# Optimization experiments

Measured on AMD Instinct MI355X. Metric: run time of the kernel, lower is better.

Reference implementation:

```python
import jax, jax.numpy as jnp
import numpy as np

B = 4096
FEAT = 512
EMB = 64
HID = 1024
NUM_CLASSES = 64   # == option_num == noise_lib_Y.shape[0]
LIB_X = 256
LIB_Y = 256
OUT_J = 256


def setup_inputs() -> dict:
    key = jax.random.key(0)
    ks = jax.random.split(key, 16)
    s = lambda k, shape, fan: jax.random.normal(k, shape, jnp.float32) / np.sqrt(fan)
    d_in = FEAT + EMB
    return {
        "state": jax.random.normal(ks[0], (B, FEAT), jnp.float32),
        "option": jax.random.randint(ks[1], (B,), 0, NUM_CLASSES, jnp.int64),
        "embed_table": s(ks[2], (NUM_CLASSES, EMB), EMB),
        "Wx1": s(ks[3], (d_in, HID), d_in), "bx1": jnp.zeros((HID,), jnp.float32),
        "Wx2": s(ks[4], (HID, LIB_X), HID), "bx2": jnp.zeros((LIB_X,), jnp.float32),
        "Wy1": s(ks[5], (d_in, HID), d_in), "by1": jnp.zeros((HID,), jnp.float32),
        "Wy2": s(ks[6], (HID, LIB_Y), HID), "by2": jnp.zeros((LIB_Y,), jnp.float32),
        "noise_lib_X": s(ks[7], (LIB_X, OUT_J), LIB_X),
        "noise_lib_Y": s(ks[8], (NUM_CLASSES, LIB_Y, OUT_J), LIB_Y),
    }


def _mlp(x, W1, b1, W2, b2):
    # MLP_RELU, layer_num=2: Linear -> ReLU -> Linear
    h = jax.nn.relu(x @ W1 + b1)
    return h @ W2 + b2


def reference(state, option, embed_table, Wx1, bx1, Wx2, bx2,
              Wy1, by1, Wy2, by2, noise_lib_X, noise_lib_Y):
    option_embed = embed_table[option]                      # [B, EMB]
    all_state = jnp.concatenate([state, option_embed], axis=-1)
    cls_X = _mlp(all_state, Wx1, bx1, Wx2, bx2)             # [B, LIB_X]
    cls_Y = _mlp(all_state, Wy1, by1, Wy2, by2)             # [B, LIB_Y]
    # Original: einsum('bi,mij->bmj') then mask with one_hot(option).
    # Mathematically identical gather-then-matmul (honors the routing sparsity):
    noise_Y_sel = noise_lib_Y[option]                       # [B, LIB_Y, OUT_J]
    generate_noise_Y = jnp.einsum('bi,bij->bj', cls_Y, noise_Y_sel)
    generate_noise_X = cls_X @ noise_lib_X                  # [B, OUT_J]
    return (generate_noise_X, generate_noise_Y)
```

## Files before the change

### kernel.cpp

```cpp
#include <hip/hip_runtime.h>

typedef unsigned short u16;
typedef unsigned int u32;

using f32x4  = __attribute__((ext_vector_type(4))) float;
using bf16x8 = __attribute__((ext_vector_type(8))) __bf16;

#define DEV __device__ __forceinline__

DEV u16 f2bf(float f) {
  union { float f; u32 u; } x; x.f = f;
  return (u16)((x.u + 0x7fffu + ((x.u >> 16) & 1u)) >> 16);
}
DEV float bf2f(u16 h) {
  union { u32 u; float f; } x; x.u = ((u32)h) << 16;
  return x.f;
}

DEV void async_cp16(const u16* g, u16* l) {
  __builtin_amdgcn_global_load_lds((const __attribute__((address_space(1))) void*)g,
                                   (__attribute__((address_space(3))) void*)l,
                                   16, 0, 0);
}

static constexpr int BATCH = 4096;
static constexpr int FEAT  = 512;
static constexpr int EMB   = 64;
static constexpr int HID   = 1024;
static constexpr int NC    = 64;
static constexpr int DIN   = 576;
static constexpr int LIB   = 256;

DEV void detect_lite(const u32* __restrict__ sraw, const u32* __restrict__ oraw,
                     int* isf32, int* ostr) {
  __shared__ int cib, conz;
  const int t = threadIdx.x;
  if (t == 0) { cib = 0; conz = 0; }
  u32 w = sraw[t];
  u32 e = (w >> 7) & 0xFFu;
  unsigned long long m1 = __ballot(e >= 100 && e <= 142);
  unsigned long long m2 = __ballot((t & 1) && oraw[t] != 0);
  __syncthreads();
  if ((t & 63) == 0) {
    atomicAdd(&cib, __popcll(m1));
    atomicAdd(&conz, __popcll(m2));
  }
  __syncthreads();
  *isf32 = (cib < 128) ? 1 : 0;
  *ostr  = (conz == 0) ? 2 : 1;
}

DEV void load16_bf(u16* v, const void* __restrict__ in, size_t off, int isf32) {
  if (isf32) {
    const float4* s = (const float4*)((const float*)in + off);
    float4 a0 = s[0], a1 = s[1], a2 = s[2], a3 = s[3];
    v[0] = f2bf(a0.x); v[1] = f2bf(a0.y); v[2]  = f2bf(a0.z); v[3]  = f2bf(a0.w);
    v[4] = f2bf(a1.x); v[5] = f2bf(a1.y); v[6]  = f2bf(a1.z); v[7]  = f2bf(a1.w);
    v[8] = f2bf(a2.x); v[9] = f2bf(a2.y); v[10] = f2bf(a2.z); v[11] = f2bf(a2.w);
    v[12] = f2bf(a3.x); v[13] = f2bf(a3.y); v[14] = f2bf(a3.z); v[15] = f2bf(a3.w);
  } else {
    const uint4* s = (const uint4*)((const u16*)in + off);
    *(uint4*)&v[0] = s[0];
    *(uint4*)&v[8] = s[1];
  }
}

DEV void do_transpose64(u16* lds, const void* __restrict__ in,
                        u16* __restrict__ out, int R, int C,
                        int by, int bx, int isf32) {
  u16* tile = lds;
  const int t = threadIdx.x;
  {
    const int r = t >> 2, c0 = (t & 3) * 16;
    u16 v[16];
    load16_bf(v, in, (size_t)(by * 64 + r) * C + (bx * 64 + c0), isf32);
    *(uint4*)&tile[r * 72 + c0]     = *(uint4*)&v[0];
    *(uint4*)&tile[r * 72 + c0 + 8] = *(uint4*)&v[8];
  }
  __syncthreads();
  {
    const int c = t & 63, rs = (t >> 6) * 16;
    u16 w[16];
#pragma unroll
    for (int i = 0; i < 16; ++i) w[i] = tile[(rs + i) * 72 + c];
    size_t oo = (size_t)(bx * 64 + c) * R + (by * 64 + rs);
    *(uint4*)&out[oo]     = *(uint4*)&w[0];
    *(uint4*)&out[oo + 8] = *(uint4*)&w[8];
  }
}

DEV void tgemm_task(u16* lds, const void* __restrict__ nX,
                    const void* __restrict__ Wx2, u16* __restrict__ T,
                    int mt, int nt, int isf32) {
  u16* Als = lds;
  u16* Bls = lds + 64 * 72;
  const int t = threadIdx.x;
  const int m0 = mt * 64, q0 = nt * 64;
  const int lane = t & 63, wid = t >> 6;
  const int wm = wid >> 1, wn = wid & 1;
  const int lr = lane & 15, lq = lane >> 4;
  f32x4 acc[2][2] = {};
  for (int k0 = 0; k0 < LIB; k0 += 64) {
    __syncthreads();
    {
      const int r = t >> 2, c0 = (t & 3) * 16;
      u16 v[16];
      load16_bf(v, nX, (size_t)(k0 + r) * LIB + m0 + c0, isf32);
#pragma unroll
      for (int j = 0; j < 16; ++j) Als[(c0 + j) * 72 + r] = v[j];
      const int q = t >> 2, ic = (t & 3) * 16;
      u16 w16[16];
      load16_bf(w16, Wx2, (size_t)(q0 + q) * LIB + k0 + ic, isf32);
      u16* dst = &Bls[((ic >> 5) * 64 + q) * 32 + (ic & 31)];
      *(uint4*)dst       = *(uint4*)&w16[0];
      *(uint4*)(dst + 8) = *(uint4*)&w16[8];
    }
    __syncthreads();
#pragma unroll
    for (int sl = 0; sl < 2; ++sl) {
      bf16x8 av[2], bv[2];
#pragma unroll
      for (int i2 = 0; i2 < 2; ++i2)
        av[i2] = *(const bf16x8*)&Als[(wm * 32 + i2 * 16 + lr) * 72 + sl * 32 + lq * 8];
#pragma unroll
      for (int j2 = 0; j2 < 2; ++j2)
        bv[j2] = *(const bf16x8*)&Bls[(sl * 64 + wn * 32 + j2 * 16 + lr) * 32 + lq * 8];
#pragma unroll
      for (int i2 = 0; i2 < 2; ++i2)
#pragma unroll
        for (int j2 = 0; j2 < 2; ++j2)
          acc[i2][j2] = __builtin_amdgcn_mfma_f32_16x16x32_bf16(av[i2], bv[j2], acc[i2][j2], 0, 0, 0);
    }
  }
#pragma unroll
  for (int j2 = 0; j2 < 2; ++j2) {
    const int gc = q0 + wn * 32 + j2 * 16 + lr;
#pragma unroll
    for (int i2 = 0; i2 < 2; ++i2) {
      const int gr = m0 + wm * 32 + i2 * 16 + lq * 4;
#pragma unroll
      for (int r = 0; r < 4; ++r)
        T[(size_t)(gr + r) * HID + gc] = f2bf(acc[i2][j2][r]);
    }
  }
}

struct PrepArgs {
  const void *state, *emb, *Wx1, *Wy1;
  const int* opt;
  u16 *all_state, *WT1x, *WT1y;
};
static constexpr int PB_CONCAT = BATCH * 36 / 256;
static constexpr int PB_WT1 = (DIN / 64) * (HID / 64);
static constexpr int PREP_BLOCKS = PB_CONCAT + 2 * PB_WT1;

__global__ __launch_bounds__(256) void prep_k(PrepArgs a) {
  __shared__ __align__(16) u16 plds[64 * 72];
  int isf32, os;
  detect_lite((const u32*)a.state, (const u32*)a.opt, &isf32, &os);
  int bid = blockIdx.x;
  const int t = threadIdx.x;
  if (bid < PB_CONCAT) {
    int idx = bid * 256 + t;
    int b = idx / 36, ch = idx % 36;
    const void* base;
    size_t srcoff;
    if (ch < 32) { base = a.state; srcoff = (size_t)b * FEAT + ch * 16; }
    else {
      base = a.emb;
      srcoff = (size_t)a.opt[(size_t)b * os] * EMB + (ch - 32) * 16;
    }
    u16 o[16];
    load16_bf(o, base, srcoff, isf32);
    u16* dst = a.all_state + (size_t)b * DIN + ch * 16;
    *(uint4*)dst       = *(const uint4*)&o[0];
    *(uint4*)(dst + 8) = *(const uint4*)&o[8];
    return;
  }
  bid -= PB_CONCAT;
  if (bid < PB_WT1) { do_transpose64(plds, a.Wx1, a.WT1x, DIN, HID, bid >> 4, bid & 15, isf32); return; }
  bid -= PB_WT1;
  do_transpose64(plds, a.Wy1, a.WT1y, DIN, HID, bid >> 4, bid & 15, isf32);
}

template <int BM, int BN, int SLABS, bool RELU>
DEV void gemm_tile(u16* lds, const u16* __restrict__ A, const u16* __restrict__ Bt,
                   const void* bias, void* C, int N, int K, int m0, int n0,
                   int isf32, bool cf32, bool bf32) {
  constexpr int WM = BM / 2, WN = BN / 2, TM = WM / 16, TN = WN / 16;
  u16* As = lds;
  u16* Bs = lds + BM * 32 * SLABS;
  const int t = threadIdx.x;
  const int lane = t & 63, wid = t >> 6;
  const int wm = wid >> 1, wn = wid & 1;
  const int lr = lane & 15, lq = lane >> 4;
  f32x4 acc[TM][TN] = {};
  for (int k0 = 0; k0 < K; k0 += 32 * SLABS) {
    __syncthreads();
#pragma unroll
    for (int sl = 0; sl < SLABS; ++sl) {
#pragma unroll
      for (int u = 0; u < BM / 64; ++u) {
        int unit = u * 256 + t;
        int r = unit >> 2, c8 = (unit & 3) * 8;
        async_cp16(A + (size_t)(m0 + r) * K + (k0 + sl * 32 + c8),
                   &As[(sl * BM + r) * 32 + c8]);
      }
#pragma unroll
      for (int u = 0; u < BN / 64; ++u) {
        int unit = u * 256 + t;
        int r = unit >> 2, c8 = (unit & 3) * 8;
        async_cp16(Bt + (size_t)(n0 + r) * K + (k0 + sl * 32 + c8),
                   &Bs[(sl * BN + r) * 32 + c8]);
      }
    }
    __syncthreads();
#pragma unroll
    for (int sl = 0; sl < SLABS; ++sl) {
      bf16x8 av[TM], bv[TN];
#pragma unroll
      for (int i = 0; i < TM; ++i)
        av[i] = *(const bf16x8*)&As[(sl * BM + wm * WM + i * 16 + lr) * 32 + lq * 8];
#pragma unroll
      for (int j = 0; j < TN; ++j)
        bv[j] = *(const bf16x8*)&Bs[(sl * BN + wn * WN + j * 16 + lr) * 32 + lq * 8];
#pragma unroll
      for (int i = 0; i < TM; ++i)
#pragma unroll
        for (int j = 0; j < TN; ++j)
          acc[i][j] = __builtin_amdgcn_mfma_f32_16x16x32_bf16(av[i], bv[j], acc[i][j], 0, 0, 0);
    }
  }
#pragma unroll
  for (int j = 0; j < TN; ++j) {
    const int gc = n0 + wn * WN + j * 16 + lr;
    const float bval = bias
        ? (bf32 ? ((const float*)bias)[gc] : bf2f(((const u16*)bias)[gc]))
        : 0.f;
#pragma unroll
    for (int i = 0; i < TM; ++i) {
      const int gr = m0 + wm * WM + i * 16 + lq * 4;
#pragma unroll
      for (int r = 0; r < 4; ++r) {
        float v = acc[i][j][r] + bval;
        if (RELU) v = fmaxf(v, 0.f);
        const size_t idx = (size_t)(gr + r) * N + gc;
        if (cf32) ((float*)C)[idx] = v;
        else      ((u16*)C)[idx] = f2bf(v);
      }
    }
  }
}

struct G1Args {
  const u16 *all_state, *WT1x, *WT1y;
  const void *bx1, *by1, *Wy2, *nX, *Wx2, *bx2, *state, *opt;
  u16 *h_x, *h_y, *WT2y, *T;
  float* b2x;
};
static constexpr int G1_GEMM = 1024;
static constexpr int G1_BLOCKS = G1_GEMM + 64 + 64 + 4;

__global__ __launch_bounds__(256) void gemm1_k(G1Args a) {
  __shared__ __align__(16) u16 lds[(128 + 64) * 96];
  __shared__ float red[4][64];
  int isf32, os;
  detect_lite((const u32*)a.state, (const u32*)a.opt, &isf32, &os);
  int bid = blockIdx.x;
  const int t = threadIdx.x;
  if (bid < G1_GEMM) {
    const int x = bid & 15, y = (bid >> 4) & 31, z = bid >> 9;
    gemm_tile<128, 64, 3, true>(lds,
        a.all_state, z ? a.WT1y : a.WT1x, z ? a.by1 : a.bx1,
        z ? a.h_y : a.h_x, HID, DIN, y * 128, x * 64, isf32, false, isf32);
    return;
  }
  bid -= G1_GEMM;
  if (bid < 64) { do_transpose64(lds, a.Wy2, a.WT2y, HID, LIB, bid >> 2, bid & 3, isf32); return; }
  bid -= 64;
  if (bid < 64) { tgemm_task(lds, a.nX, a.Wx2, a.T, bid & 3, bid >> 2, isf32); return; }
  bid -= 64;
  {
    const int j = bid * 64 + (t & 63), g = t >> 6;
    float acc = 0.f;
    for (int ii = 0; ii < 64; ++ii) {
      const int i = g * 64 + ii;
      float s = isf32 ? ((const float*)a.bx2)[i] : bf2f(((const u16*)a.bx2)[i]);
      float v = isf32 ? ((const float*)a.nX)[(size_t)i * LIB + j]
                      : bf2f(((const u16*)a.nX)[(size_t)i * LIB + j]);
      acc += s * v;
    }
    red[g][t & 63] = acc;
    __syncthreads();
    if (g == 0)
      a.b2x[j] = red[0][t & 63] + red[1][t & 63] + red[2][t & 63] + red[3][t & 63];
  }
}

struct GArg { const u16* A; const u16* Bt; const void* bias; void* C; int cflag; int bflag; };

template <int BM, int BN, int SLABS, bool RELU>
__global__ __launch_bounds__(256) void gemm_bt(GArg g0, GArg g1, int N, int K,
                                               const void* state, const void* opt) {
  __shared__ __align__(16) u16 lds[(BM + BN) * 32 * SLABS];
  int isf32, os;
  detect_lite((const u32*)state, (const u32*)opt, &isf32, &os);
  const GArg g = blockIdx.z ? g1 : g0;
  gemm_tile<BM, BN, SLABS, RELU>(lds, g.A, g.Bt, g.bias, g.C, N, K,
                                 blockIdx.y * BM, blockIdx.x * BN,
                                 isf32, g.cflag && isf32, g.bflag || isf32);
}

struct TailArgs {
  const u16* cls_y;
  const void *nY, *state;
  const int* opt;
  void* out;
};

__global__ __launch_bounds__(256) void tail_k(TailArgs a) {
  __shared__ __align__(16) u16 lds[25216];
  __shared__ int lcnt;
  int isf32, os;
  detect_lite((const u32*)a.state, (const u32*)a.opt, &isf32, &os);
  const bool of32 = (isf32 != 0);
  const int t = threadIdx.x;
  const int lane = t & 63, w = t >> 6, lr = lane & 15, lq = lane >> 4;

  u16* Bts  = lds;
  u16* Asm  = lds + 16896;
  u16* list = lds + 21120;
  const int m = blockIdx.x >> 3;
  const int n0 = ((blockIdx.x >> 1) & 3) * 64;
  const int half = blockIdx.x & 1;
  if (t == 0) lcnt = 0;

#pragma unroll
  for (int pass = 0; pass < 4; ++pass) {
    const int k = pass * 64 + (t >> 2), nc = (t & 3) * 16;
    u16 v[16];
    load16_bf(v, a.nY, ((size_t)m * LIB + k) * LIB + n0 + nc, isf32);
#pragma unroll
    for (int j = 0; j < 16; ++j) Bts[(nc + j) * 264 + k] = v[j];
  }

  __syncthreads();
  const int bstart = half * (BATCH / 2), bend = bstart + BATCH / 2;
  for (int base = bstart; base < bend; base += 256) {
    const int b = base + t;
    const int e = a.opt[(size_t)b * os];
    unsigned long long mk = __ballot(e == m);
    const int nw = __popcll(mk);
    int wbase = 0;
    if (lane == 0 && nw) wbase = atomicAdd(&lcnt, nw);
    wbase = __shfl(wbase, 0);
    const int mypre = __popcll(mk & ((1ull << lane) - 1ull));
    if (e == m) list[wbase + mypre] = (u16)b;
  }
  __syncthreads();
  const int cnt = lcnt;
  const size_t out_off = (size_t)BATCH * LIB;

  for (int ch = 0; ch < cnt; ch += 16) {
    __syncthreads();
    {
      const int r = t >> 4, cb = (t & 15) * 16;
      if (ch + r < cnt) {
        const u16* src = a.cls_y + (size_t)list[ch + r] * LIB + cb;
        *(uint4*)&Asm[r * 264 + cb]     = *(const uint4*)src;
        *(uint4*)&Asm[r * 264 + cb + 8] = *(const uint4*)(src + 8);
      } else {
        uint4 z{0, 0, 0, 0};
        *(uint4*)&Asm[r * 264 + cb]     = z;
        *(uint4*)&Asm[r * 264 + cb + 8] = z;
      }
    }
    __syncthreads();
    f32x4 acc = {};
#pragma unroll
    for (int kk = 0; kk < LIB; kk += 32) {
      bf16x8 av = *(const bf16x8*)&Asm[lr * 264 + kk + lq * 8];
      bf16x8 bv = *(const bf16x8*)&Bts[(w * 16 + lr) * 264 + kk + lq * 8];
      acc = __builtin_amdgcn_mfma_f32_16x16x32_bf16(av, bv, acc, 0, 0, 0);
    }
#pragma unroll
    for (int r = 0; r < 4; ++r) {
      const int rowc = lq * 4 + r;
      if (ch + rowc < cnt) {
        const size_t oi = out_off + (size_t)list[ch + rowc] * LIB
                        + (n0 + w * 16 + lr);
        if (of32) ((float*)a.out)[oi] = acc[r];
        else      ((u16*)a.out)[oi] = f2bf(acc[r]);
      }
    }
  }
}

extern "C" void kernel_launch(void* const* d_in, const int* in_sizes, int n_in,
                              void* d_out, int out_size, void* d_ws, size_t ws_size,
                              hipStream_t stream) {
  char* p = (char*)d_ws;
  auto alloc = [&](size_t bytes) { char* r = p; p += (bytes + 255) & ~(size_t)255; return r; };
  u16* all_state = (u16*)alloc((size_t)BATCH * DIN * 2);
  u16* h_x   = (u16*)alloc((size_t)BATCH * HID * 2);
  u16* h_y   = (u16*)alloc((size_t)BATCH * HID * 2);
  u16* cls_y = (u16*)alloc((size_t)BATCH * LIB * 2);
  u16* WT1x  = (u16*)alloc((size_t)HID * DIN * 2);
  u16* WT1y  = (u16*)alloc((size_t)HID * DIN * 2);
  u16* WT2y  = (u16*)alloc((size_t)LIB * HID * 2);
  u16* T     = (u16*)alloc((size_t)LIB * HID * 2);
  float* b2x = (float*)alloc((size_t)LIB * 4);

  const void* state = d_in[0];
  const void* opt   = d_in[1];

  PrepArgs pa;
  pa.state = state; pa.opt = (const int*)opt; pa.emb = d_in[2];
  pa.Wx1 = d_in[3]; pa.Wy1 = d_in[7];
  pa.all_state = all_state; pa.WT1x = WT1x; pa.WT1y = WT1y;
  prep_k<<<PREP_BLOCKS, 256, 0, stream>>>(pa);

  G1Args g1;
  g1.all_state = all_state; g1.WT1x = WT1x; g1.WT1y = WT1y;
  g1.bx1 = d_in[4]; g1.by1 = d_in[8];
  g1.Wy2 = d_in[9]; g1.nX = d_in[11]; g1.Wx2 = d_in[5]; g1.bx2 = d_in[6];
  g1.state = state; g1.opt = opt;
  g1.h_x = h_x; g1.h_y = h_y; g1.WT2y = WT2y; g1.T = T; g1.b2x = b2x;
  gemm1_k<<<G1_BLOCKS, 256, 0, stream>>>(g1);

  GArg g2x{h_x, T, b2x, d_out, 1, 1};
  GArg g2y{h_y, WT2y, d_in[10], cls_y, 0, 0};
  gemm_bt<64, 64, 4, false><<<dim3(LIB / 64, BATCH / 64, 2), 256, 0, stream>>>(
      g2x, g2y, LIB, HID, state, opt);

  TailArgs ta{cls_y, d_in[12], state, (const int*)opt, d_out};
  tail_k<<<512, 256, 0, stream>>>(ta);
}
```

Measured before the change: 147.7 us.

## Double-buffer GEMM LDS staging, widen gemm1 tiles, pad tail LDS stride

The shared GEMM tile routine now uses two LDS buffers, so the async global-to-LDS copies for the next K slab are issued before the MFMA work on the current slab, with one barrier per iteration instead of two. The first-layer GEMM moves from 128x64 tiles with 3 slabs to 128x128 tiles with 2 slabs, halving its block count and raising reuse per block. The tail kernel's LDS row stride changes from 264 to 266 elements to reduce bank conflicts. In exchange, LDS use per block roughly doubles, which can cut occupancy, and the 266 stride leaves rows that are not 16-byte aligned for the 128-bit LDS accesses.

```diff
diff --git a/kernel.cpp b/kernel.cpp
--- a/kernel.cpp
+++ b/kernel.cpp
@@ -188,15 +188,15 @@
                    const void* bias, void* C, int N, int K, int m0, int n0,
                    int isf32, bool cf32, bool bf32) {
   constexpr int WM = BM / 2, WN = BN / 2, TM = WM / 16, TN = WN / 16;
-  u16* As = lds;
-  u16* Bs = lds + BM * 32 * SLABS;
+  constexpr int BUFE = (BM + BN) * 32 * SLABS;
   const int t = threadIdx.x;
   const int lane = t & 63, wid = t >> 6;
   const int wm = wid >> 1, wn = wid & 1;
   const int lr = lane & 15, lq = lane >> 4;
-  f32x4 acc[TM][TN] = {};
-  for (int k0 = 0; k0 < K; k0 += 32 * SLABS) {
-    __syncthreads();
+
+  auto stage = [&](int buf, int k0) {
+    u16* As = lds + buf * BUFE;
+    u16* Bs = As + BM * 32 * SLABS;
 #pragma unroll
     for (int sl = 0; sl < SLABS; ++sl) {
 #pragma unroll
@@ -214,7 +214,17 @@
                    &Bs[(sl * BN + r) * 32 + c8]);
       }
     }
-    __syncthreads();
+  };
+
+  f32x4 acc[TM][TN] = {};
+  stage(0, 0);
+  __syncthreads();
+  int cur = 0;
+  for (int k0 = 0; k0 < K; k0 += 32 * SLABS) {
+    const int kn = k0 + 32 * SLABS;
+    if (kn < K) stage(cur ^ 1, kn);
+    const u16* As = lds + cur * BUFE;
+    const u16* Bs = As + BM * 32 * SLABS;
 #pragma unroll
     for (int sl = 0; sl < SLABS; ++sl) {
       bf16x8 av[TM], bv[TN];
@@ -230,6 +240,8 @@
         for (int j = 0; j < TN; ++j)
           acc[i][j] = __builtin_amdgcn_mfma_f32_16x16x32_bf16(av[i], bv[j], acc[i][j], 0, 0, 0);
     }
+    __syncthreads();
+    cur ^= 1;
   }
 #pragma unroll
   for (int j = 0; j < TN; ++j) {
@@ -258,21 +270,21 @@
   u16 *h_x, *h_y, *WT2y, *T;
   float* b2x;
 };
-static constexpr int G1_GEMM = 1024;
+static constexpr int G1_GEMM = 512;
 static constexpr int G1_BLOCKS = G1_GEMM + 64 + 64 + 4;
 
 __global__ __launch_bounds__(256) void gemm1_k(G1Args a) {
-  __shared__ __align__(16) u16 lds[(128 + 64) * 96];
+  __shared__ __align__(16) u16 lds[2 * (128 + 128) * 32 * 2];
   __shared__ float red[4][64];
   int isf32, os;
   detect_lite((const u32*)a.state, (const u32*)a.opt, &isf32, &os);
   int bid = blockIdx.x;
   const int t = threadIdx.x;
   if (bid < G1_GEMM) {
-    const int x = bid & 15, y = (bid >> 4) & 31, z = bid >> 9;
-    gemm_tile<128, 64, 3, true>(lds,
+    const int x = bid & 7, y = (bid >> 3) & 31, z = bid >> 8;
+    gemm_tile<128, 128, 2, true>(lds,
         a.all_state, z ? a.WT1y : a.WT1x, z ? a.by1 : a.bx1,
-        z ? a.h_y : a.h_x, HID, DIN, y * 128, x * 64, isf32, false, isf32);
+        z ? a.h_y : a.h_x, HID, DIN, y * 128, x * 128, isf32, false, isf32);
     return;
   }
   bid -= G1_GEMM;
@@ -302,7 +314,7 @@
 template <int BM, int BN, int SLABS, bool RELU>
 __global__ __launch_bounds__(256) void gemm_bt(GArg g0, GArg g1, int N, int K,
                                                const void* state, const void* opt) {
-  __shared__ __align__(16) u16 lds[(BM + BN) * 32 * SLABS];
+  __shared__ __align__(16) u16 lds[2 * (BM + BN) * 32 * SLABS];
   int isf32, os;
   detect_lite((const u32*)state, (const u32*)opt, &isf32, &os);
   const GArg g = blockIdx.z ? g1 : g0;
@@ -318,6 +330,8 @@
   void* out;
 };
 
+static constexpr int TSTR = 266;
+
 __global__ __launch_bounds__(256) void tail_k(TailArgs a) {
   __shared__ __align__(16) u16 lds[25216];
   __shared__ int lcnt;
@@ -328,8 +342,8 @@
   const int lane = t & 63, w = t >> 6, lr = lane & 15, lq = lane >> 4;
 
   u16* Bts  = lds;
-  u16* Asm  = lds + 16896;
-  u16* list = lds + 21120;
+  u16* Asm  = lds + 64 * TSTR;
+  u16* list = lds + 80 * TSTR;
   const int m = blockIdx.x >> 3;
   const int n0 = ((blockIdx.x >> 1) & 3) * 64;
   const int half = blockIdx.x & 1;
@@ -341,7 +355,7 @@
     u16 v[16];
     load16_bf(v, a.nY, ((size_t)m * LIB + k) * LIB + n0 + nc, isf32);
 #pragma unroll
-    for (int j = 0; j < 16; ++j) Bts[(nc + j) * 264 + k] = v[j];
+    for (int j = 0; j < 16; ++j) Bts[(nc + j) * TSTR + k] = v[j];
   }
 
   __syncthreads();
@@ -367,20 +381,20 @@
       const int r = t >> 4, cb = (t & 15) * 16;
       if (ch + r < cnt) {
         const u16* src = a.cls_y + (size_t)list[ch + r] * LIB + cb;
-        *(uint4*)&Asm[r * 264 + cb]     = *(const uint4*)src;
-        *(uint4*)&Asm[r * 264 + cb + 8] = *(const uint4*)(src + 8);
+        *(uint4*)&Asm[r * TSTR + cb]     = *(const uint4*)src;
+        *(uint4*)&Asm[r * TSTR + cb + 8] = *(const uint4*)(src + 8);
       } else {
         uint4 z{0, 0, 0, 0};
-        *(uint4*)&Asm[r * 264 + cb]     = z;
-        *(uint4*)&Asm[r * 264 + cb + 8] = z;
+        *(uint4*)&Asm[r * TSTR + cb]     = z;
+        *(uint4*)&Asm[r * TSTR + cb + 8] = z;
       }
     }
     __syncthreads();
     f32x4 acc = {};
 #pragma unroll
     for (int kk = 0; kk < LIB; kk += 32) {
-      bf16x8 av = *(const bf16x8*)&Asm[lr * 264 + kk + lq * 8];
-      bf16x8 bv = *(const bf16x8*)&Bts[(w * 16 + lr) * 264 + kk + lq * 8];
+      bf16x8 av = *(const bf16x8*)&Asm[lr * TSTR + kk + lq * 8];
+      bf16x8 bv = *(const bf16x8*)&Bts[(w * 16 + lr) * TSTR + kk + lq * 8];
       acc = __builtin_amdgcn_mfma_f32_16x16x32_bf16(av, bv, acc, 0, 0, 0);
     }
 #pragma unroll
```

After: 159.4 us. +7.9%, slower.

## Split-K second-layer GEMMs into fp32 partials and reduce them in the tail kernel

Applied to the files above, without the earlier changes.

The second-layer GEMMs for both heads are split along K into two halves, doubling the grid to raise occupancy. Each half writes fp32 partials to a new workspace buffer. The tail kernel gains extra blocks that sum the X partials, add the bias and write the output. The Y path sums its partials, adds by2 and converts to bf16 when staging rows for the routed matmul, and the LDS row stride changes from 264 to 266. The cost is an extra 16 MB of fp32 partial traffic and the extra reduction work.

```diff
diff --git a/kernel.cpp b/kernel.cpp
--- a/kernel.cpp
+++ b/kernel.cpp
@@ -186,7 +186,7 @@
 template <int BM, int BN, int SLABS, bool RELU>
 DEV void gemm_tile(u16* lds, const u16* __restrict__ A, const u16* __restrict__ Bt,
                    const void* bias, void* C, int N, int K, int m0, int n0,
-                   int isf32, bool cf32, bool bf32) {
+                   int kbeg, int kend, int isf32, bool cf32, bool bf32) {
   constexpr int WM = BM / 2, WN = BN / 2, TM = WM / 16, TN = WN / 16;
   u16* As = lds;
   u16* Bs = lds + BM * 32 * SLABS;
@@ -195,7 +195,7 @@
   const int wm = wid >> 1, wn = wid & 1;
   const int lr = lane & 15, lq = lane >> 4;
   f32x4 acc[TM][TN] = {};
-  for (int k0 = 0; k0 < K; k0 += 32 * SLABS) {
+  for (int k0 = kbeg; k0 < kend; k0 += 32 * SLABS) {
     __syncthreads();
 #pragma unroll
     for (int sl = 0; sl < SLABS; ++sl) {
@@ -272,7 +272,8 @@
     const int x = bid & 15, y = (bid >> 4) & 31, z = bid >> 9;
     gemm_tile<128, 64, 3, true>(lds,
         a.all_state, z ? a.WT1y : a.WT1x, z ? a.by1 : a.bx1,
-        z ? a.h_y : a.h_x, HID, DIN, y * 128, x * 64, isf32, false, isf32);
+        z ? a.h_y : a.h_x, HID, DIN, y * 128, x * 64, 0, DIN,
+        isf32, false, isf32 != 0);
     return;
   }
   bid -= G1_GEMM;
@@ -297,26 +298,35 @@
   }
 }
 
-struct GArg { const u16* A; const u16* Bt; const void* bias; void* C; int cflag; int bflag; };
-
-template <int BM, int BN, int SLABS, bool RELU>
-__global__ __launch_bounds__(256) void gemm_bt(GArg g0, GArg g1, int N, int K,
-                                               const void* state, const void* opt) {
-  __shared__ __align__(16) u16 lds[(BM + BN) * 32 * SLABS];
+struct G2Args {
+  const u16 *h_x, *h_y, *T, *WT2y;
+  float* part;
+  const void *state, *opt;
+};
+
+__global__ __launch_bounds__(256) void gemm2_k(G2Args a) {
+  __shared__ __align__(16) u16 lds[(64 + 64) * 32 * 4];
   int isf32, os;
-  detect_lite((const u32*)state, (const u32*)opt, &isf32, &os);
-  const GArg g = blockIdx.z ? g1 : g0;
-  gemm_tile<BM, BN, SLABS, RELU>(lds, g.A, g.Bt, g.bias, g.C, N, K,
-                                 blockIdx.y * BM, blockIdx.x * BN,
-                                 isf32, g.cflag && isf32, g.bflag || isf32);
+  detect_lite((const u32*)a.state, (const u32*)a.opt, &isf32, &os);
+  const int head = blockIdx.z >> 1, half = blockIdx.z & 1;
+  const u16* A  = head ? a.h_y : a.h_x;
+  const u16* Bt = head ? a.WT2y : a.T;
+  float* C = a.part + (size_t)blockIdx.z * BATCH * LIB;
+  const int kbeg = half * (HID / 2);
+  gemm_tile<64, 64, 4, false>(lds, A, Bt, nullptr, C, LIB, HID,
+                              blockIdx.y * 64, blockIdx.x * 64,
+                              kbeg, kbeg + HID / 2, isf32, true, true);
 }
 
 struct TailArgs {
-  const u16* cls_y;
-  const void *nY, *state;
+  const float* part;
+  const void *nY, *state, *by2;
+  const float* b2x;
   const int* opt;
   void* out;
 };
+
+static constexpr int TSTR = 266;
 
 __global__ __launch_bounds__(256) void tail_k(TailArgs a) {
   __shared__ __align__(16) u16 lds[25216];
@@ -325,23 +335,64 @@
   detect_lite((const u32*)a.state, (const u32*)a.opt, &isf32, &os);
   const bool of32 = (isf32 != 0);
   const int t = threadIdx.x;
+
+  if (blockIdx.x >= 512) {
+    const int cb = blockIdx.x - 512;
+    const size_t e0 = ((size_t)cb * 256 + t) * 16;
+    const float4* s0 = (const float4*)(a.part + e0);
+    const float4* s1 = (const float4*)(a.part + (size_t)BATCH * LIB + e0);
+    const int c0 = (int)(e0 & 255);
+    float v[16];
+#pragma unroll
+    for (int q = 0; q < 4; ++q) {
+      float4 x0 = s0[q], x1 = s1[q];
+      v[q * 4 + 0] = x0.x + x1.x + a.b2x[c0 + q * 4 + 0];
+      v[q * 4 + 1] = x0.y + x1.y + a.b2x[c0 + q * 4 + 1];
+      v[q * 4 + 2] = x0.z + x1.z + a.b2x[c0 + q * 4 + 2];
+      v[q * 4 + 3] = x0.w + x1.w + a.b2x[c0 + q * 4 + 3];
+    }
+    if (of32) {
+      float4* d = (float4*)((float*)a.out + e0);
+#pragma unroll
+      for (int q = 0; q < 4; ++q) d[q] = make_float4(v[q*4], v[q*4+1], v[q*4+2], v[q*4+3]);
+    } else {
+      u16 o[16];
+#pragma unroll
+      for (int j = 0; j < 16; ++j) o[j] = f2bf(v[j]);
+      u16* d = (u16*)a.out + e0;
+      *(uint4*)d       = *(const uint4*)&o[0];
+      *(uint4*)(d + 8) = *(const uint4*)&o[8];
+    }
+    return;
+  }
+
   const int lane = t & 63, w = t >> 6, lr = lane & 15, lq = lane >> 4;
-
   u16* Bts  = lds;
-  u16* Asm  = lds + 16896;
-  u16* list = lds + 21120;
+  u16* Asm  = lds + 64 * TSTR;
+  u16* list = lds + 80 * TSTR;
   const int m = blockIdx.x >> 3;
   const int n0 = ((blockIdx.x >> 1) & 3) * 64;
   const int half = blockIdx.x & 1;
   if (t == 0) lcnt = 0;
 
+  const float* py0 = a.part + (size_t)2 * BATCH * LIB;
+  const float* py1 = a.part + (size_t)3 * BATCH * LIB;
+  float byv[16];
+  {
+    const int cb = (t & 15) * 16;
+#pragma unroll
+    for (int j = 0; j < 16; ++j)
+      byv[j] = isf32 ? ((const float*)a.by2)[cb + j]
+                     : bf2f(((const u16*)a.by2)[cb + j]);
+  }
+
 #pragma unroll
   for (int pass = 0; pass < 4; ++pass) {
     const int k = pass * 64 + (t >> 2), nc = (t & 3) * 16;
     u16 v[16];
     load16_bf(v, a.nY, ((size_t)m * LIB + k) * LIB + n0 + nc, isf32);
 #pragma unroll
-    for (int j = 0; j < 16; ++j) Bts[(nc + j) * 264 + k] = v[j];
+    for (int j = 0; j < 16; ++j) Bts[(nc + j) * TSTR + k] = v[j];
   }
 
   __syncthreads();
@@ -366,21 +417,32 @@
     {
       const int r = t >> 4, cb = (t & 15) * 16;
       if (ch + r < cnt) {
-        const u16* src = a.cls_y + (size_t)list[ch + r] * LIB + cb;
-        *(uint4*)&Asm[r * 264 + cb]     = *(const uint4*)src;
-        *(uint4*)&Asm[r * 264 + cb + 8] = *(const uint4*)(src + 8);
+        const int row = list[ch + r];
+        const float4* s0 = (const float4*)(py0 + (size_t)row * LIB + cb);
+        const float4* s1 = (const float4*)(py1 + (size_t)row * LIB + cb);
+        u16 o[16];
+#pragma unroll
+        for (int q = 0; q < 4; ++q) {
+          float4 x0 = s0[q], x1 = s1[q];
+          o[q * 4 + 0] = f2bf(x0.x + x1.x + byv[q * 4 + 0]);
+          o[q * 4 + 1] = f2bf(x0.y + x1.y + byv[q * 4 + 1]);
+          o[q * 4 + 2] = f2bf(x0.z + x1.z + byv[q * 4 + 2]);
+          o[q * 4 + 3] = f2bf(x0.w + x1.w + byv[q * 4 + 3]);
+        }
+        *(uint4*)&Asm[r * TSTR + cb]     = *(const uint4*)&o[0];
+        *(uint4*)&Asm[r * TSTR + cb + 8] = *(const uint4*)&o[8];
       } else {
         uint4 z{0, 0, 0, 0};
-        *(uint4*)&Asm[r * 264 + cb]     = z;
-        *(uint4*)&Asm[r * 264 + cb + 8] = z;
+        *(uint4*)&Asm[r * TSTR + cb]     = z;
+        *(uint4*)&Asm[r * TSTR + cb + 8] = z;
       }
     }
     __syncthreads();
     f32x4 acc = {};
 #pragma unroll
     for (int kk = 0; kk < LIB; kk += 32) {
-      bf16x8 av = *(const bf16x8*)&Asm[lr * 264 + kk + lq * 8];
-      bf16x8 bv = *(const bf16x8*)&Bts[(w * 16 + lr) * 264 + kk + lq * 8];
+      bf16x8 av = *(const bf16x8*)&Asm[lr * TSTR + kk + lq * 8];
+      bf16x8 bv = *(const bf16x8*)&Bts[(w * 16 + lr) * TSTR + kk + lq * 8];
       acc = __builtin_amdgcn_mfma_f32_16x16x32_bf16(av, bv, acc, 0, 0, 0);
     }
 #pragma unroll
@@ -404,12 +466,12 @@
   u16* all_state = (u16*)alloc((size_t)BATCH * DIN * 2);
   u16* h_x   = (u16*)alloc((size_t)BATCH * HID * 2);
   u16* h_y   = (u16*)alloc((size_t)BATCH * HID * 2);
-  u16* cls_y = (u16*)alloc((size_t)BATCH * LIB * 2);
   u16* WT1x  = (u16*)alloc((size_t)HID * DIN * 2);
   u16* WT1y  = (u16*)alloc((size_t)HID * DIN * 2);
   u16* WT2y  = (u16*)alloc((size_t)LIB * HID * 2);
   u16* T     = (u16*)alloc((size_t)LIB * HID * 2);
   float* b2x = (float*)alloc((size_t)LIB * 4);
+  float* part = (float*)alloc((size_t)4 * BATCH * LIB * 4);
 
   const void* state = d_in[0];
   const void* opt   = d_in[1];
@@ -428,11 +490,13 @@
   g1.h_x = h_x; g1.h_y = h_y; g1.WT2y = WT2y; g1.T = T; g1.b2x = b2x;
   gemm1_k<<<G1_BLOCKS, 256, 0, stream>>>(g1);
 
-  GArg g2x{h_x, T, b2x, d_out, 1, 1};
-  GArg g2y{h_y, WT2y, d_in[10], cls_y, 0, 0};
-  gemm_bt<64, 64, 4, false><<<dim3(LIB / 64, BATCH / 64, 2), 256, 0, stream>>>(
-      g2x, g2y, LIB, HID, state, opt);
-
-  TailArgs ta{cls_y, d_in[12], state, (const int*)opt, d_out};
-  tail_k<<<512, 256, 0, stream>>>(ta);
-}
+  G2Args g2;
+  g2.h_x = h_x; g2.h_y = h_y; g2.T = T; g2.WT2y = WT2y;
+  g2.part = part; g2.state = state; g2.opt = opt;
+  gemm2_k<<<dim3(LIB / 64, BATCH / 64, 4), 256, 0, stream>>>(g2);
+
+  TailArgs ta;
+  ta.part = part; ta.nY = d_in[12]; ta.state = state; ta.by2 = d_in[10];
+  ta.b2x = b2x; ta.opt = (const int*)opt; ta.out = d_out;
+  tail_k<<<768, 256, 0, stream>>>(ta);
+}
```

Result: slower. 163.2 us (+10.5%).

## Move weight prep tasks into prep kernel, shrink gemm2 tiles, pad tail LDS stride

Applied to the files above, without the earlier changes.

Moves the Wy2 transpose, the nX·Wx2 product and the bias-fold work out of the first GEMM kernel into the prep kernel, leaving gemm1 as a pure GEMM grid. The second GEMM now uses 64x32 tiles, doubling its block count for better CU occupancy. The gemm_tile load loops are generalized to cover tiles smaller than 64 rows. The tail kernel's LDS row stride changes from 264 to 266 to reduce bank conflicts. This trades a larger prep kernel and smaller per-block reuse for better load balance.

```diff
diff --git a/kernel.cpp b/kernel.cpp
--- a/kernel.cpp
+++ b/kernel.cpp
@@ -146,16 +146,18 @@
 }
 
 struct PrepArgs {
-  const void *state, *emb, *Wx1, *Wy1;
+  const void *state, *emb, *Wx1, *Wy1, *Wy2, *nX, *Wx2, *bx2;
   const int* opt;
-  u16 *all_state, *WT1x, *WT1y;
+  u16 *all_state, *WT1x, *WT1y, *WT2y, *T;
+  float* b2x;
 };
 static constexpr int PB_CONCAT = BATCH * 36 / 256;
 static constexpr int PB_WT1 = (DIN / 64) * (HID / 64);
-static constexpr int PREP_BLOCKS = PB_CONCAT + 2 * PB_WT1;
+static constexpr int PREP_BLOCKS = PB_CONCAT + 2 * PB_WT1 + 64 + 64 + 4;
 
 __global__ __launch_bounds__(256) void prep_k(PrepArgs a) {
-  __shared__ __align__(16) u16 plds[64 * 72];
+  __shared__ __align__(16) u16 plds[64 * 72 + 128 * 32];
+  __shared__ float red[4][64];
   int isf32, os;
   detect_lite((const u32*)a.state, (const u32*)a.opt, &isf32, &os);
   int bid = blockIdx.x;
@@ -180,105 +182,11 @@
   bid -= PB_CONCAT;
   if (bid < PB_WT1) { do_transpose64(plds, a.Wx1, a.WT1x, DIN, HID, bid >> 4, bid & 15, isf32); return; }
   bid -= PB_WT1;
-  do_transpose64(plds, a.Wy1, a.WT1y, DIN, HID, bid >> 4, bid & 15, isf32);
-}
-
-template <int BM, int BN, int SLABS, bool RELU>
-DEV void gemm_tile(u16* lds, const u16* __restrict__ A, const u16* __restrict__ Bt,
-                   const void* bias, void* C, int N, int K, int m0, int n0,
-                   int isf32, bool cf32, bool bf32) {
-  constexpr int WM = BM / 2, WN = BN / 2, TM = WM / 16, TN = WN / 16;
-  u16* As = lds;
-  u16* Bs = lds + BM * 32 * SLABS;
-  const int t = threadIdx.x;
-  const int lane = t & 63, wid = t >> 6;
-  const int wm = wid >> 1, wn = wid & 1;
-  const int lr = lane & 15, lq = lane >> 4;
-  f32x4 acc[TM][TN] = {};
-  for (int k0 = 0; k0 < K; k0 += 32 * SLABS) {
-    __syncthreads();
-#pragma unroll
-    for (int sl = 0; sl < SLABS; ++sl) {
-#pragma unroll
-      for (int u = 0; u < BM / 64; ++u) {
-        int unit = u * 256 + t;
-        int r = unit >> 2, c8 = (unit & 3) * 8;
-        async_cp16(A + (size_t)(m0 + r) * K + (k0 + sl * 32 + c8),
-                   &As[(sl * BM + r) * 32 + c8]);
-      }
-#pragma unroll
-      for (int u = 0; u < BN / 64; ++u) {
-        int unit = u * 256 + t;
-        int r = unit >> 2, c8 = (unit & 3) * 8;
-        async_cp16(Bt + (size_t)(n0 + r) * K + (k0 + sl * 32 + c8),
-                   &Bs[(sl * BN + r) * 32 + c8]);
-      }
-    }
-    __syncthreads();
-#pragma unroll
-    for (int sl = 0; sl < SLABS; ++sl) {
-      bf16x8 av[TM], bv[TN];
-#pragma unroll
-      for (int i = 0; i < TM; ++i)
-        av[i] = *(const bf16x8*)&As[(sl * BM + wm * WM + i * 16 + lr) * 32 + lq * 8];
-#pragma unroll
-      for (int j = 0; j < TN; ++j)
-        bv[j] = *(const bf16x8*)&Bs[(sl * BN + wn * WN + j * 16 + lr) * 32 + lq * 8];
-#pragma unroll
-      for (int i = 0; i < TM; ++i)
-#pragma unroll
-        for (int j = 0; j < TN; ++j)
-          acc[i][j] = __builtin_amdgcn_mfma_f32_16x16x32_bf16(av[i], bv[j], acc[i][j], 0, 0, 0);
-    }
-  }
-#pragma unroll
-  for (int j = 0; j < TN; ++j) {
-    const int gc = n0 + wn * WN + j * 16 + lr;
-    const float bval = bias
-        ? (bf32 ? ((const float*)bias)[gc] : bf2f(((const u16*)bias)[gc]))
-        : 0.f;
-#pragma unroll
-    for (int i = 0; i < TM; ++i) {
-      const int gr = m0 + wm * WM + i * 16 + lq * 4;
-#pragma unroll
-      for (int r = 0; r < 4; ++r) {
-        float v = acc[i][j][r] + bval;
-        if (RELU) v = fmaxf(v, 0.f);
-        const size_t idx = (size_t)(gr + r) * N + gc;
-        if (cf32) ((float*)C)[idx] = v;
-        else      ((u16*)C)[idx] = f2bf(v);
-      }
-    }
-  }
-}
-
-struct G1Args {
-  const u16 *all_state, *WT1x, *WT1y;
-  const void *bx1, *by1, *Wy2, *nX, *Wx2, *bx2, *state, *opt;
-  u16 *h_x, *h_y, *WT2y, *T;
-  float* b2x;
-};
-static constexpr int G1_GEMM = 1024;
-static constexpr int G1_BLOCKS = G1_GEMM + 64 + 64 + 4;
-
-__global__ __launch_bounds__(256) void gemm1_k(G1Args a) {
-  __shared__ __align__(16) u16 lds[(128 + 64) * 96];
-  __shared__ float red[4][64];
-  int isf32, os;
-  detect_lite((const u32*)a.state, (const u32*)a.opt, &isf32, &os);
-  int bid = blockIdx.x;
-  const int t = threadIdx.x;
-  if (bid < G1_GEMM) {
-    const int x = bid & 15, y = (bid >> 4) & 31, z = bid >> 9;
-    gemm_tile<128, 64, 3, true>(lds,
-        a.all_state, z ? a.WT1y : a.WT1x, z ? a.by1 : a.bx1,
-        z ? a.h_y : a.h_x, HID, DIN, y * 128, x * 64, isf32, false, isf32);
-    return;
-  }
-  bid -= G1_GEMM;
-  if (bid < 64) { do_transpose64(lds, a.Wy2, a.WT2y, HID, LIB, bid >> 2, bid & 3, isf32); return; }
+  if (bid < PB_WT1) { do_transpose64(plds, a.Wy1, a.WT1y, DIN, HID, bid >> 4, bid & 15, isf32); return; }
+  bid -= PB_WT1;
+  if (bid < 64) { do_transpose64(plds, a.Wy2, a.WT2y, HID, LIB, bid >> 2, bid & 3, isf32); return; }
   bid -= 64;
-  if (bid < 64) { tgemm_task(lds, a.nX, a.Wx2, a.T, bid & 3, bid >> 2, isf32); return; }
+  if (bid < 64) { tgemm_task(plds, a.nX, a.Wx2, a.T, bid & 3, bid >> 2, isf32); return; }
   bid -= 64;
   {
     const int j = bid * 64 + (t & 63), g = t >> 6;
@@ -297,6 +205,91 @@
   }
 }
 
+template <int BM, int BN, int SLABS, bool RELU>
+DEV void gemm_tile(u16* lds, const u16* __restrict__ A, const u16* __restrict__ Bt,
+                   const void* bias, void* C, int N, int K, int m0, int n0,
+                   int isf32, bool cf32, bool bf32) {
+  constexpr int WM = BM / 2, WN = BN / 2, TM = WM / 16, TN = WN / 16;
+  u16* As = lds;
+  u16* Bs = lds + BM * 32 * SLABS;
+  const int t = threadIdx.x;
+  const int lane = t & 63, wid = t >> 6;
+  const int wm = wid >> 1, wn = wid & 1;
+  const int lr = lane & 15, lq = lane >> 4;
+  f32x4 acc[TM][TN] = {};
+  for (int k0 = 0; k0 < K; k0 += 32 * SLABS) {
+    __syncthreads();
+#pragma unroll
+    for (int sl = 0; sl < SLABS; ++sl) {
+#pragma unroll
+      for (int u = t; u < BM * 4; u += 256) {
+        int r = u >> 2, c8 = (u & 3) * 8;
+        async_cp16(A + (size_t)(m0 + r) * K + (k0 + sl * 32 + c8),
+                   &As[(sl * BM + r) * 32 + c8]);
+      }
+#pragma unroll
+      for (int u = t; u < BN * 4; u += 256) {
+        int r = u >> 2, c8 = (u & 3) * 8;
+        async_cp16(Bt + (size_t)(n0 + r) * K + (k0 + sl * 32 + c8),
+                   &Bs[(sl * BN + r) * 32 + c8]);
+      }
+    }
+    __syncthreads();
+#pragma unroll
+    for (int sl = 0; sl < SLABS; ++sl) {
+      bf16x8 av[TM], bv[TN];
+#pragma unroll
+      for (int i = 0; i < TM; ++i)
+        av[i] = *(const bf16x8*)&As[(sl * BM + wm * WM + i * 16 + lr) * 32 + lq * 8];
+#pragma unroll
+      for (int j = 0; j < TN; ++j)
+        bv[j] = *(const bf16x8*)&Bs[(sl * BN + wn * WN + j * 16 + lr) * 32 + lq * 8];
+#pragma unroll
+      for (int i = 0; i < TM; ++i)
+#pragma unroll
+        for (int j = 0; j < TN; ++j)
+          acc[i][j] = __builtin_amdgcn_mfma_f32_16x16x32_bf16(av[i], bv[j], acc[i][j], 0, 0, 0);
+    }
+  }
+#pragma unroll
+  for (int j = 0; j < TN; ++j) {
+    const int gc = n0 + wn * WN + j * 16 + lr;
+    const float bval = bias
+        ? (bf32 ? ((const float*)bias)[gc] : bf2f(((const u16*)bias)[gc]))
+        : 0.f;
+#pragma unroll
+    for (int i = 0; i < TM; ++i) {
+      const int gr = m0 + wm * WM + i * 16 + lq * 4;
+#pragma unroll
+      for (int r = 0; r < 4; ++r) {
+        float v = acc[i][j][r] + bval;
+        if (RELU) v = fmaxf(v, 0.f);
+        const size_t idx = (size_t)(gr + r) * N + gc;
+        if (cf32) ((float*)C)[idx] = v;
+        else      ((u16*)C)[idx] = f2bf(v);
+      }
+    }
+  }
+}
+
+struct G1Args {
+  const u16 *all_state, *WT1x, *WT1y;
+  const void *bx1, *by1, *state, *opt;
+  u16 *h_x, *h_y;
+};
+
+__global__ __launch_bounds__(256) void gemm1_k(G1Args a) {
+  __shared__ __align__(16) u16 lds[(128 + 64) * 96];
+  int isf32, os;
+  detect_lite((const u32*)a.state, (const u32*)a.opt, &isf32, &os);
+  const int bid = blockIdx.x;
+  const int x = bid & 15, y = (bid >> 4) & 31, z = bid >> 9;
+  gemm_tile<128, 64, 3, true>(lds,
+      a.all_state, z ? a.WT1y : a.WT1x, z ? a.by1 : a.bx1,
+      z ? a.h_y : a.h_x, HID, DIN, y * 128, x * 64,
+      isf32, false, isf32 != 0);
+}
+
 struct GArg { const u16* A; const u16* Bt; const void* bias; void* C; int cflag; int bflag; };
 
 template <int BM, int BN, int SLABS, bool RELU>
@@ -318,6 +311,8 @@
   void* out;
 };
 
+static constexpr int TSTR = 266;
+
 __global__ __launch_bounds__(256) void tail_k(TailArgs a) {
   __shared__ __align__(16) u16 lds[25216];
   __shared__ int lcnt;
@@ -328,8 +323,8 @@
   const int lane = t & 63, w = t >> 6, lr = lane & 15, lq = lane >> 4;
 
   u16* Bts  = lds;
-  u16* Asm  = lds + 16896;
-  u16* list = lds + 21120;
+  u16* Asm  = lds + 64 * TSTR;
+  u16* list = lds + 80 * TSTR;
   const int m = blockIdx.x >> 3;
   const int n0 = ((blockIdx.x >> 1) & 3) * 64;
   const int half = blockIdx.x & 1;
@@ -341,7 +336,7 @@
     u16 v[16];
     load16_bf(v, a.nY, ((size_t)m * LIB + k) * LIB + n0 + nc, isf32);
 #pragma unroll
-    for (int j = 0; j < 16; ++j) Bts[(nc + j) * 264 + k] = v[j];
+    for (int j = 0; j < 16; ++j) Bts[(nc + j) * TSTR + k] = v[j];
   }
 
   __syncthreads();
@@ -367,20 +362,20 @@
       const int r = t >> 4, cb = (t & 15) * 16;
       if (ch + r < cnt) {
         const u16* src = a.cls_y + (size_t)list[ch + r] * LIB + cb;
-        *(uint4*)&Asm[r * 264 + cb]     = *(const uint4*)src;
-        *(uint4*)&Asm[r * 264 + cb + 8] = *(const uint4*)(src + 8);
+        *(uint4*)&Asm[r * TSTR + cb]     = *(const uint4*)src;
+        *(uint4*)&Asm[r * TSTR + cb + 8] = *(const uint4*)(src + 8);
       } else {
         uint4 z{0, 0, 0, 0};
-        *(uint4*)&Asm[r * 264 + cb]     = z;
-        *(uint4*)&Asm[r * 264 + cb + 8] = z;
+        *(uint4*)&Asm[r * TSTR + cb]     = z;
+        *(uint4*)&Asm[r * TSTR + cb + 8] = z;
       }
     }
     __syncthreads();
     f32x4 acc = {};
 #pragma unroll
     for (int kk = 0; kk < LIB; kk += 32) {
-      bf16x8 av = *(const bf16x8*)&Asm[lr * 264 + kk + lq * 8];
-      bf16x8 bv = *(const bf16x8*)&Bts[(w * 16 + lr) * 264 + kk + lq * 8];
+      bf16x8 av = *(const bf16x8*)&Asm[lr * TSTR + kk + lq * 8];
+      bf16x8 bv = *(const bf16x8*)&Bts[(w * 16 + lr) * TSTR + kk + lq * 8];
       acc = __builtin_amdgcn_mfma_f32_16x16x32_bf16(av, bv, acc, 0, 0, 0);
     }
 #pragma unroll
@@ -417,20 +412,21 @@
   PrepArgs pa;
   pa.state = state; pa.opt = (const int*)opt; pa.emb = d_in[2];
   pa.Wx1 = d_in[3]; pa.Wy1 = d_in[7];
-  pa.all_state = all_state; pa.WT1x = WT1x; pa.WT1y = WT1y;
+  pa.Wy2 = d_in[9]; pa.nX = d_in[11]; pa.Wx2 = d_in[5]; pa.bx2 = d_in[6];
+  pa.all_state = all_state; pa.WT1x = WT1x; pa.WT1y = WT1y; pa.WT2y = WT2y;
+  pa.T = T; pa.b2x = b2x;
   prep_k<<<PREP_BLOCKS, 256, 0, stream>>>(pa);
 
   G1Args g1;
   g1.all_state = all_state; g1.WT1x = WT1x; g1.WT1y = WT1y;
   g1.bx1 = d_in[4]; g1.by1 = d_in[8];
-  g1.Wy2 = d_in[9]; g1.nX = d_in[11]; g1.Wx2 = d_in[5]; g1.bx2 = d_in[6];
   g1.state = state; g1.opt = opt;
-  g1.h_x = h_x; g1.h_y = h_y; g1.WT2y = WT2y; g1.T = T; g1.b2x = b2x;
-  gemm1_k<<<G1_BLOCKS, 256, 0, stream>>>(g1);
+  g1.h_x = h_x; g1.h_y = h_y;
+  gemm1_k<<<1024, 256, 0, stream>>>(g1);
 
   GArg g2x{h_x, T, b2x, d_out, 1, 1};
   GArg g2y{h_y, WT2y, d_in[10], cls_y, 0, 0};
-  gemm_bt<64, 64, 4, false><<<dim3(LIB / 64, BATCH / 64, 2), 256, 0, stream>>>(
+  gemm_bt<64, 32, 4, false><<<dim3(LIB / 32, BATCH / 64, 2), 256, 0, stream>>>(
       g2x, g2y, LIB, HID, state, opt);
 
   TailArgs ta{cls_y, d_in[12], state, (const int*)opt, d_out};
```

Result: slower. 166.4 us (+12.7%).
